# Kernel tuning notes

Hardware: AMD Instinct MI355X
Metric: run time of the kernel (lower is better)

## Reference

```python
import jax, jax.numpy as jnp
import numpy as np

N_HEADS = 16
HEAD_DIM = 128  # d_model // n_heads


def rope(x):
    # x: [B, H, T, D]. Matches the torch module: interleaved even/odd split,
    # then concat([x1*cos - x2*sin, x1*sin + x2*cos], axis=-1).
    T, D = x.shape[2], x.shape[3]
    inv_freq = 1.0 / (10000.0 ** (jnp.arange(0, D, 2, dtype=x.dtype) / D))  # [D/2]
    freqs = jnp.arange(T, dtype=x.dtype)[:, None] * inv_freq[None, :]       # [T, D/2]
    sin, cos = jnp.sin(freqs), jnp.cos(freqs)                               # [T, D/2]
    x1, x2 = x[..., ::2], x[..., 1::2]                                      # [B,H,T,D/2]
    return jnp.concatenate([x1 * cos - x2 * sin, x1 * sin + x2 * cos], axis=-1)


def setup_inputs() -> dict:
    key = jax.random.key(0)
    ks = jax.random.split(key, 5)
    B, T, C = 2, 2048, 2048
    scale = 1.0 / np.sqrt(C)
    return {
        "x": jax.random.normal(ks[0], (B, T, C), dtype=jnp.float32),
        "W_qkv": jax.random.normal(ks[1], (3 * C, C), dtype=jnp.float32) * scale,
        "b_qkv": jnp.zeros((3 * C,), dtype=jnp.float32),
        "W_out": jax.random.normal(ks[2], (C, C), dtype=jnp.float32) * scale,
        "b_out": jnp.zeros((C,), dtype=jnp.float32),
    }


def reference(x, W_qkv, b_qkv, W_out, b_out):
    B, T, C = x.shape
    H, D = N_HEADS, HEAD_DIM
    qkv = x @ W_qkv.T + b_qkv                      # [B, T, 3C]
    qkv = qkv.reshape(B, T, 3, H, D)
    q, k, v = qkv[:, :, 0], qkv[:, :, 1], qkv[:, :, 2]  # [B, T, H, D]
    q = rope(jnp.transpose(q, (0, 2, 1, 3)))       # [B, H, T, D]
    k = rope(jnp.transpose(k, (0, 2, 1, 3)))
    v = jnp.transpose(v, (0, 2, 1, 3))
    scores = jnp.einsum("bhqd,bhkd->bhqk", q, k) / jnp.sqrt(jnp.asarray(D, x.dtype))
    causal = jnp.tril(jnp.ones((T, T), dtype=bool))
    scores = jnp.where(causal, scores, jnp.finfo(x.dtype).min)
    attn = jax.nn.softmax(scores, axis=-1)
    out = jnp.einsum("bhqk,bhkd->bhqd", attn, v)   # [B, H, T, D]
    out = jnp.transpose(out, (0, 2, 1, 3)).reshape(B, T, C)
    return out @ W_out.T + b_out
```

## Files before the change

### kernel.cpp

```cpp
#include <hip/hip_runtime.h>
#include <hip/hip_bf16.h>

typedef __attribute__((ext_vector_type(8))) short bf16x8;
typedef __attribute__((ext_vector_type(4))) float f32x4;

#define GLOAD_LDS16(gptr, lptr) \
  __builtin_amdgcn_global_load_lds((const __attribute__((address_space(1))) void*)(gptr), \
                                   (__attribute__((address_space(3))) void*)(lptr), 16, 0, 0)

__device__ __forceinline__ unsigned short f2b(float f) {
  union { float f; unsigned u; } x; x.f = f;
  unsigned r = x.u + 0x7fffu + ((x.u >> 16) & 1u);
  return (unsigned short)(r >> 16);
}
__device__ __forceinline__ float b2f(unsigned short u) {
  union { unsigned u; float f; } x; x.u = ((unsigned)u) << 16;
  return x.f;
}
__device__ __forceinline__ unsigned cvt_pk_bf16(float lo, float hi) {
  unsigned d;
  asm("v_cvt_pk_bf16_f32 %0, %1, %2" : "=v"(d) : "v"(lo), "v"(hi));
  return d;
}

__global__ void cast_kernel(const float* __restrict__ in, unsigned short* __restrict__ out, int n) {
  const int i = (blockIdx.x * 256 + threadIdx.x) * 4;
  if (i < n) {
    const float4 v = *(const float4*)(in + i);
    ushort4 r;
    r.x = f2b(v.x); r.y = f2b(v.y); r.z = f2b(v.z); r.w = f2b(v.w);
    *(ushort4*)(out + i) = r;
  }
}

template<int OUTF32>
__global__ __launch_bounds__(512, 4)
void gemm128(const unsigned short* __restrict__ A,
             const unsigned short* __restrict__ Bm,
             const float* __restrict__ bias,
             void* __restrict__ Cp,
             int M, int N, int K)
{
  __shared__ __align__(16) char Lds[73728];
  const int t  = threadIdx.x;
  const int l  = t & 63;
  const int w  = t >> 6;
  const int lr = l & 15;
  const int lkb = (l >> 4) << 4;
  const int wr = w >> 2;
  const int wc = w & 3;

  const int nwg = gridDim.x;
  const int wg  = (blockIdx.x & 7) * (nwg >> 3) + (blockIdx.x >> 3);
  const int NBN = N >> 8;
  const int bm = wg / NBN, bn = wg % NBN;

  const long K2 = (long)K * 2;
  const char* Ab = (const char*)A  + (long)(bm * 128) * K2;
  const char* Bb = (const char*)Bm + (long)(bn * 256) * K2;

  auto swz = [](int a) -> int { return a ^ (((a >> 7) & 3) << 4); };

  const int t16 = t << 4;
  const int da  = swz(t16);
  const long sa = (long)(da >> 6) * K2 + (da & 63);
  const int db0 = swz(t16), db1 = swz(8192 + t16);
  const long sb0 = (long)(db0 >> 6) * K2 + (db0 & 63);
  const long sb1 = (long)(db1 >> 6) * K2 + (db1 & 63);

  auto stage = [&](int g) {
    char* S = Lds + (g % 3) * 24576;
    const char* As = Ab + (long)g * 64;
    const char* Bs = Bb + (long)g * 64;
    GLOAD_LDS16(As + sa,  S + t16);
    GLOAD_LDS16(Bs + sb0, S + 8192 + t16);
    GLOAD_LDS16(Bs + sb1, S + 16384 + t16);
  };

  int aoff[4], boff[4];
#pragma unroll
  for (int mi = 0; mi < 4; ++mi) {
    const int a = ((wr * 64 + mi * 16 + lr) << 6) | lkb;
    aoff[mi] = swz(a);
  }
#pragma unroll
  for (int ni = 0; ni < 4; ++ni) {
    const int a = ((wc * 64 + ni * 16 + lr) << 6) | lkb;
    boff[ni] = 8192 + swz(a);
  }

  f32x4 acc[4][4] = {};
  const int NT = K >> 5;
  bf16x8 af[4], bfr[4];

  stage(0); stage(1);
  asm volatile("s_waitcnt vmcnt(3)" ::: "memory");
  __builtin_amdgcn_s_barrier();
  __builtin_amdgcn_sched_barrier(0);
#pragma unroll
  for (int mi = 0; mi < 4; ++mi) af[mi]  = *(const bf16x8*)(Lds + aoff[mi]);
#pragma unroll
  for (int ni = 0; ni < 4; ++ni) bfr[ni] = *(const bf16x8*)(Lds + boff[ni]);

  for (int tt = 0; tt < NT; ++tt) {
    if (tt + 2 < NT) stage(tt + 2);
    __builtin_amdgcn_s_setprio(1);
#pragma unroll
    for (int mi = 0; mi < 4; ++mi)
#pragma unroll
      for (int ni = 0; ni < 4; ++ni)
        acc[mi][ni] = __builtin_amdgcn_mfma_f32_16x16x32_bf16(af[mi], bfr[ni], acc[mi][ni], 0, 0, 0);
    __builtin_amdgcn_s_setprio(0);
    if (tt + 1 < NT) {
      if (tt + 2 < NT) asm volatile("s_waitcnt vmcnt(3)" ::: "memory");
      else             asm volatile("s_waitcnt vmcnt(0)" ::: "memory");
      __builtin_amdgcn_s_barrier();
      __builtin_amdgcn_sched_barrier(0);
      const char* S = Lds + ((tt + 1) % 3) * 24576;
#pragma unroll
      for (int mi = 0; mi < 4; ++mi) af[mi]  = *(const bf16x8*)(S + aoff[mi]);
#pragma unroll
      for (int ni = 0; ni < 4; ++ni) bfr[ni] = *(const bf16x8*)(S + boff[ni]);
    }
  }

  const int roff = (l >> 4) << 2;
  const int row0 = bm * 128 + wr * 64 + roff;
  const int col0 = bn * 256 + wc * 64 + lr;
  float bv[4];
#pragma unroll
  for (int ni = 0; ni < 4; ++ni) bv[ni] = bias ? bias[col0 + ni * 16] : 0.0f;
#pragma unroll
  for (int mi = 0; mi < 4; ++mi) {
#pragma unroll
    for (int r = 0; r < 4; ++r) {
      const long rb = (long)(row0 + mi * 16 + r) * N;
#pragma unroll
      for (int ni = 0; ni < 4; ++ni) {
        const float v = acc[mi][ni][r] + bv[ni];
        if (OUTF32) ((float*)Cp)[rb + col0 + ni * 16] = v;
        else ((unsigned short*)Cp)[rb + col0 + ni * 16] = f2b(v);
      }
    }
  }
}

__global__ void prep_kernel(const unsigned short* __restrict__ qkv,
                            unsigned short* __restrict__ Qr,
                            unsigned short* __restrict__ Kr,
                            unsigned short* __restrict__ Vt)
{
  const int T = 2048;
  __shared__ unsigned short ld[128][65];
  const int bh = blockIdx.y, tb = blockIdx.x;
  const int b = bh >> 4, h = bh & 15;
  const int t = threadIdx.x;

#pragma unroll
  for (int i = 0; i < 16; ++i) {
    const int idx = i * 256 + t;
    const int d  = idx & 63;
    const int tt = tb * 64 + (idx >> 6);
    const long base = ((long)(b * T + tt) * 3) * 2048 + h * 128;
    const float inv = exp2f(-(float)d * 0.2076205059304602f);
    const float fr = (float)tt * inv;
    float sn, cs;
    sincosf(fr, &sn, &cs);
    const float q1 = b2f(qkv[base + 2 * d]);
    const float q2 = b2f(qkv[base + 2 * d + 1]);
    const float k1 = b2f(qkv[base + 2048 + 2 * d]);
    const float k2 = b2f(qkv[base + 2048 + 2 * d + 1]);
    const long ob = ((long)bh * T + tt) * 128;
    Qr[ob + d]      = f2b(q1 * cs - q2 * sn);
    Qr[ob + 64 + d] = f2b(q1 * sn + q2 * cs);
    Kr[ob + d]      = f2b(k1 * cs - k2 * sn);
    Kr[ob + 64 + d] = f2b(k1 * sn + k2 * cs);
  }

#pragma unroll
  for (int i = 0; i < 32; ++i) {
    const int idx = i * 256 + t;
    const int d = idx & 127, tr = idx >> 7;
    ld[d][tr] = qkv[((long)(b * T + tb * 64 + tr) * 3 + 2) * 2048 + h * 128 + d];
  }
  __syncthreads();
#pragma unroll
  for (int i = 0; i < 32; ++i) {
    const int idx = i * 256 + t;
    const int tc = idx & 63, dr = idx >> 6;
    Vt[((long)bh * 128 + dr) * T + tb * 64 + tc] = ld[dr][tc];
  }
}

__global__ __launch_bounds__(256)
void attn_fwd(const unsigned short* __restrict__ Q,
              const unsigned short* __restrict__ Kg,
              const unsigned short* __restrict__ Vt,
              unsigned short* __restrict__ O, int T)
{
  __shared__ __align__(16) unsigned short Ks[2][64 * 128];
  __shared__ __align__(16) unsigned short Vs[2][128 * 64];
  const int t = threadIdx.x;
  const int w = t >> 6, l = t & 63;
  const int lr = l & 15;
  const int g  = l >> 4;
  const int g16 = g << 4;
  const int sw = (lr & 7) << 4;
  const int bh = blockIdx.x;
  const int qt = (gridDim.y - 1) - blockIdx.y;
  const int q0 = qt * 64 + w * 16;
  const long hbase = (long)bh * T * 128;
  const long hbase2 = hbase * 2;
  const long T2 = (long)T * 2;
  const int roff = g << 2;
  const float C1 = 0.08838834764831845f * 1.4426950408889634f;

  bf16x8 qf[4];
  const unsigned short* Qrow = Q + hbase + (long)(q0 + lr) * 128;
#pragma unroll
  for (int ds = 0; ds < 4; ++ds) qf[ds] = *(const bf16x8*)&Qrow[ds * 32 + (g16 >> 1)];

  f32x4 o[8] = {};
  float m = -INFINITY, lsum = 0.f;

  auto stage = [&](int kt, int buf) {
#pragma unroll
    for (int c = 0; c < 4; ++c) {
      const int o2 = t * 16 + c * 4096;
      const int krow = o2 >> 8, kcb = o2 & 255;
      GLOAD_LDS16((const char*)Kg + hbase2 + (long)kt * 16384 + krow * 256 + (kcb ^ ((krow & 7) << 4)),
                  (char*)Ks[buf] + o2);
      const int vrow = o2 >> 7, vcb = o2 & 127;
      GLOAD_LDS16((const char*)Vt + (long)(bh * 128 + vrow) * T2 + (long)kt * 128 + (vcb ^ ((vrow & 7) << 4)),
                  (char*)Vs[buf] + o2);
    }
  };

  const int ntile = qt + 1;
  stage(0, 0);
  __syncthreads();

  for (int kt = 0; kt < ntile; ++kt) {
    const int cur = kt & 1;
    if (kt + 1 < ntile) stage(kt + 1, cur ^ 1);

    const char* KsB = (const char*)Ks[cur];
    const char* VsB = (const char*)Vs[cur];

    f32x4 s[4] = {};
    __builtin_amdgcn_s_setprio(1);
#pragma unroll
    for (int tj = 0; tj < 4; ++tj)
#pragma unroll
      for (int ds = 0; ds < 4; ++ds) {
        bf16x8 kf = *(const bf16x8*)(KsB + (tj * 16 + lr) * 256 + ((ds * 64 + g16) ^ sw));
        s[tj] = __builtin_amdgcn_mfma_f32_16x16x32_bf16(kf, qf[ds], s[tj], 0, 0, 0);
      }
    __builtin_amdgcn_s_setprio(0);

    if (kt == qt) {
#pragma unroll
      for (int tj = 0; tj < 4; ++tj)
#pragma unroll
        for (int r = 0; r < 4; ++r)
          if (kt * 64 + tj * 16 + 4 * g + r > q0 + lr) s[tj][r] = -INFINITY;
    }

    float pmax = -INFINITY;
#pragma unroll
    for (int tj = 0; tj < 4; ++tj)
#pragma unroll
      for (int r = 0; r < 4; ++r) pmax = fmaxf(pmax, s[tj][r]);
    pmax = fmaxf(pmax, __shfl_xor(pmax, 16, 64));
    pmax = fmaxf(pmax, __shfl_xor(pmax, 32, 64));
    const float mn = fmaxf(m, pmax * C1);
    const float corr = exp2f(m - mn);
    m = mn;

    float p[4][4];
    float rs = 0.f;
#pragma unroll
    for (int tj = 0; tj < 4; ++tj)
#pragma unroll
      for (int r = 0; r < 4; ++r) {
        const float pv = exp2f(fmaf(s[tj][r], C1, -mn));
        p[tj][r] = pv;
        rs += pv;
      }
    rs += __shfl_xor(rs, 16, 64);
    rs += __shfl_xor(rs, 32, 64);
    lsum = lsum * corr + rs;

    unsigned D8[4][2];
#pragma unroll
    for (int tj = 0; tj < 4; ++tj) {
      D8[tj][0] = cvt_pk_bf16(p[tj][0], p[tj][1]);
      D8[tj][1] = cvt_pk_bf16(p[tj][2], p[tj][3]);
    }

    float corrj[4];
#pragma unroll
    for (int j = 0; j < 4; ++j) corrj[j] = __shfl(corr, roff + j, 64);
#pragma unroll
    for (int nj = 0; nj < 8; ++nj)
#pragma unroll
      for (int j = 0; j < 4; ++j) o[nj][j] *= corrj[j];

    __builtin_amdgcn_s_setprio(1);
#pragma unroll
    for (int ks = 0; ks < 2; ++ks) {
      union { unsigned u[4]; bf16x8 v; } pfu;
#pragma unroll
      for (int k2 = 0; k2 < 4; ++k2) {
        const int src = lr | ((2 * (g & 1) + (k2 >> 1)) << 4);
        const unsigned dwA = __shfl(D8[2 * ks][k2 & 1], src, 64);
        const unsigned dwB = __shfl(D8[2 * ks + 1][k2 & 1], src, 64);
        pfu.u[k2] = (g & 2) ? dwB : dwA;
      }
#pragma unroll
      for (int nj = 0; nj < 8; ++nj) {
        bf16x8 vf = *(const bf16x8*)(VsB + (nj * 16 + lr) * 128 + ((ks * 64 + g16) ^ sw));
        o[nj] = __builtin_amdgcn_mfma_f32_16x16x32_bf16(pfu.v, vf, o[nj], 0, 0, 0);
      }
    }
    __builtin_amdgcn_s_setprio(0);
    __syncthreads();
  }

  const float inv = 1.0f / lsum;
  float invj[4];
#pragma unroll
  for (int j = 0; j < 4; ++j) invj[j] = __shfl(inv, roff + j, 64);
  const int b = bh >> 4, h = bh & 15;
#pragma unroll
  for (int nj = 0; nj < 8; ++nj)
#pragma unroll
    for (int j = 0; j < 4; ++j) {
      const int q = q0 + roff + j;
      const int d = nj * 16 + lr;
      O[(long)(b * T + q) * 2048 + h * 128 + d] = f2b(o[nj][j] * invj[j]);
    }
}

extern "C" void kernel_launch(void* const* d_in, const int* in_sizes, int n_in,
                              void* d_out, int out_size, void* d_ws, size_t ws_size,
                              hipStream_t stream)
{
  const int B = 2, T = 2048, C = 2048;
  const int M = B * T;
  const int N1 = 3 * C;
  const float* x    = (const float*)d_in[0];
  const float* Wqkv = (const float*)d_in[1];
  const float* bqkv = (const float*)d_in[2];
  const float* Wout = (const float*)d_in[3];
  const float* bout = (const float*)d_in[4];
  float* out = (float*)d_out;

  char* p = (char*)d_ws;
  unsigned short* xb    = (unsigned short*)p; p += (size_t)M * C * 2;
  unsigned short* wqkvb = (unsigned short*)p; p += (size_t)N1 * C * 2;
  unsigned short* woutb = (unsigned short*)p; p += (size_t)C * C * 2;
  unsigned short* qkv   = (unsigned short*)p; p += (size_t)M * N1 * 2;
  unsigned short* Qr    = (unsigned short*)p; p += (size_t)M * C * 2;
  unsigned short* Kr    = (unsigned short*)p; p += (size_t)M * C * 2;
  unsigned short* Vt    = (unsigned short*)p; p += (size_t)M * C * 2;
  unsigned short* Ob    = xb;

  cast_kernel<<<M * C / 1024, 256, 0, stream>>>(x, xb, M * C);
  cast_kernel<<<N1 * C / 1024, 256, 0, stream>>>(Wqkv, wqkvb, N1 * C);
  cast_kernel<<<C * C / 1024, 256, 0, stream>>>(Wout, woutb, C * C);

  gemm128<0><<<dim3((M / 128) * (N1 / 256)), 512, 0, stream>>>(xb, wqkvb, bqkv, qkv, M, N1, C);

  prep_kernel<<<dim3(T / 64, 32), 256, 0, stream>>>(qkv, Qr, Kr, Vt);

  attn_fwd<<<dim3(32, T / 64), 256, 0, stream>>>(Qr, Kr, Vt, Ob, T);

  gemm128<1><<<dim3((M / 128) * (C / 256)), 512, 0, stream>>>(Ob, woutb, bout, out, M, C, C);
}
```

Measured before the change: 290.8 us.

## Merge cast kernels, single-buffer V with explicit waitcnt, lazy softmax rescale

```diff
diff --git a/kernel.cpp b/kernel.cpp
--- a/kernel.cpp
+++ b/kernel.cpp
@@ -23,14 +23,22 @@
   return d;
 }
 
-__global__ void cast_kernel(const float* __restrict__ in, unsigned short* __restrict__ out, int n) {
-  const int i = (blockIdx.x * 256 + threadIdx.x) * 4;
-  if (i < n) {
-    const float4 v = *(const float4*)(in + i);
-    ushort4 r;
-    r.x = f2b(v.x); r.y = f2b(v.y); r.z = f2b(v.z); r.w = f2b(v.w);
-    *(ushort4*)(out + i) = r;
-  }
+__global__ void cast3_kernel(const float* __restrict__ x,
+                             const float* __restrict__ wq,
+                             const float* __restrict__ wo,
+                             unsigned short* __restrict__ out)
+{
+  const long n1 = 8388608L;
+  const long n2 = 20971520L;
+  const long i = ((long)blockIdx.x * 256 + threadIdx.x) * 4;
+  const float* src; long off;
+  if (i < n1)      { src = x;  off = i; }
+  else if (i < n2) { src = wq; off = i - n1; }
+  else             { src = wo; off = i - n2; }
+  const float4 v = *(const float4*)(src + off);
+  ushort4 r;
+  r.x = f2b(v.x); r.y = f2b(v.y); r.z = f2b(v.z); r.w = f2b(v.w);
+  *(ushort4*)(out + i) = r;
 }
 
 template<int OUTF32>
@@ -199,7 +207,7 @@
               unsigned short* __restrict__ O, int T)
 {
   __shared__ __align__(16) unsigned short Ks[2][64 * 128];
-  __shared__ __align__(16) unsigned short Vs[2][128 * 64];
+  __shared__ __align__(16) unsigned short Vs[128 * 64];
   const int t = threadIdx.x;
   const int w = t >> 6, l = t & 63;
   const int lr = l & 15;
@@ -223,29 +231,35 @@
   f32x4 o[8] = {};
   float m = -INFINITY, lsum = 0.f;
 
-  auto stage = [&](int kt, int buf) {
+  auto stageK = [&](int kt, int buf) {
 #pragma unroll
     for (int c = 0; c < 4; ++c) {
       const int o2 = t * 16 + c * 4096;
       const int krow = o2 >> 8, kcb = o2 & 255;
       GLOAD_LDS16((const char*)Kg + hbase2 + (long)kt * 16384 + krow * 256 + (kcb ^ ((krow & 7) << 4)),
                   (char*)Ks[buf] + o2);
+    }
+  };
+  auto stageV = [&](int kt) {
+#pragma unroll
+    for (int c = 0; c < 4; ++c) {
+      const int o2 = t * 16 + c * 4096;
       const int vrow = o2 >> 7, vcb = o2 & 127;
       GLOAD_LDS16((const char*)Vt + (long)(bh * 128 + vrow) * T2 + (long)kt * 128 + (vcb ^ ((vrow & 7) << 4)),
-                  (char*)Vs[buf] + o2);
+                  (char*)Vs + o2);
     }
   };
 
   const int ntile = qt + 1;
-  stage(0, 0);
+  stageK(0, 0);
+  stageV(0);
   __syncthreads();
 
   for (int kt = 0; kt < ntile; ++kt) {
     const int cur = kt & 1;
-    if (kt + 1 < ntile) stage(kt + 1, cur ^ 1);
+    if (kt + 1 < ntile) stageK(kt + 1, cur ^ 1);
 
     const char* KsB = (const char*)Ks[cur];
-    const char* VsB = (const char*)Vs[cur];
 
     f32x4 s[4] = {};
     __builtin_amdgcn_s_setprio(1);
@@ -273,9 +287,15 @@
       for (int r = 0; r < 4; ++r) pmax = fmaxf(pmax, s[tj][r]);
     pmax = fmaxf(pmax, __shfl_xor(pmax, 16, 64));
     pmax = fmaxf(pmax, __shfl_xor(pmax, 32, 64));
-    const float mn = fmaxf(m, pmax * C1);
-    const float corr = exp2f(m - mn);
-    m = mn;
+    const float pm = pmax * C1;
+
+    const bool need = !__all(pm - m <= 8.0f);
+    float corr = 1.0f;
+    if (need) {
+      const float mn = fmaxf(m, pm);
+      corr = exp2f(m - mn);
+      m = mn;
+    }
 
     float p[4][4];
     float rs = 0.f;
@@ -283,7 +303,7 @@
     for (int tj = 0; tj < 4; ++tj)
 #pragma unroll
       for (int r = 0; r < 4; ++r) {
-        const float pv = exp2f(fmaf(s[tj][r], C1, -mn));
+        const float pv = exp2f(fmaf(s[tj][r], C1, -m));
         p[tj][r] = pv;
         rs += pv;
       }
@@ -298,13 +318,20 @@
       D8[tj][1] = cvt_pk_bf16(p[tj][2], p[tj][3]);
     }
 
-    float corrj[4];
-#pragma unroll
-    for (int j = 0; j < 4; ++j) corrj[j] = __shfl(corr, roff + j, 64);
-#pragma unroll
-    for (int nj = 0; nj < 8; ++nj)
-#pragma unroll
-      for (int j = 0; j < 4; ++j) o[nj][j] *= corrj[j];
+    if (need) {
+      float corrj[4];
+#pragma unroll
+      for (int j = 0; j < 4; ++j) corrj[j] = __shfl(corr, roff + j, 64);
+#pragma unroll
+      for (int nj = 0; nj < 8; ++nj)
+#pragma unroll
+        for (int j = 0; j < 4; ++j) o[nj][j] *= corrj[j];
+    }
+
+    if (kt + 1 < ntile) asm volatile("s_waitcnt vmcnt(4)" ::: "memory");
+    else                asm volatile("s_waitcnt vmcnt(0)" ::: "memory");
+    __builtin_amdgcn_s_barrier();
+    __builtin_amdgcn_sched_barrier(0);
 
     __builtin_amdgcn_s_setprio(1);
 #pragma unroll
@@ -319,12 +346,14 @@
       }
 #pragma unroll
       for (int nj = 0; nj < 8; ++nj) {
-        bf16x8 vf = *(const bf16x8*)(VsB + (nj * 16 + lr) * 128 + ((ks * 64 + g16) ^ sw));
+        bf16x8 vf = *(const bf16x8*)((const char*)Vs + (nj * 16 + lr) * 128 + ((ks * 64 + g16) ^ sw));
         o[nj] = __builtin_amdgcn_mfma_f32_16x16x32_bf16(pfu.v, vf, o[nj], 0, 0, 0);
       }
     }
     __builtin_amdgcn_s_setprio(0);
+
     __syncthreads();
+    if (kt + 1 < ntile) stageV(kt + 1);
   }
 
   const float inv = 1.0f / lsum;
@@ -366,9 +395,8 @@
   unsigned short* Vt    = (unsigned short*)p; p += (size_t)M * C * 2;
   unsigned short* Ob    = xb;
 
-  cast_kernel<<<M * C / 1024, 256, 0, stream>>>(x, xb, M * C);
-  cast_kernel<<<N1 * C / 1024, 256, 0, stream>>>(Wqkv, wqkvb, N1 * C);
-  cast_kernel<<<C * C / 1024, 256, 0, stream>>>(Wout, woutb, C * C);
+  const long ncast = (long)M * C + (long)N1 * C + (long)C * C;
+  cast3_kernel<<<(int)(ncast / 1024), 256, 0, stream>>>(x, Wqkv, Wout, xb);
 
   gemm128<0><<<dim3((M / 128) * (N1 / 256)), 512, 0, stream>>>(xb, wqkvb, bqkv, qkv, M, N1, C);
 
```

After: 286.5 us. About the same (-1.5%).
